# Kernel tuning notes

Measured on AMD Instinct MI355X. Metric: run time of the kernel, lower is better.

The kernel has to match this reference:

```python
import jax, jax.numpy as jnp
import numpy as np

NEG_INF = -1e30  # stand-in for -inf that stays stable under softmax


def setup_inputs() -> dict:
    key = jax.random.key(0)
    kk, kq, kv, ko = jax.random.split(key, 4)
    B, S, D = 4, 2048, 512
    return {
        "keys": jax.random.normal(kk, (B, S, D), dtype=jnp.float32),
        "queries": jax.random.normal(kq, (B, S, D), dtype=jnp.float32),
        "values": jax.random.normal(kv, (B, S, D), dtype=jnp.float32),
        "original": jax.random.normal(ko, (B, S, D), dtype=jnp.float32),
    }


def reference(keys, queries, values, original):
    # logits[b, i, j] = q[b, i, :] . k[b, j, :]  (no 1/sqrt(d) scaling in source)
    logits = jnp.einsum("bqd,bkd->bqk", queries, keys)
    S = logits.shape[-1]
    # causal mask: -inf strictly above the diagonal (triu, k=1)
    causal = jnp.tril(jnp.ones((S, S), dtype=bool))  # True where allowed
    logits = jnp.where(causal[None, :, :], logits, NEG_INF)
    probs = jax.nn.softmax(logits, axis=-1)
    read = jnp.einsum("bqk,bkd->bqd", probs, values)
    return jnp.concatenate([original, read], axis=-1)  # [B, S, 2D]
```

## Files before the change

### kernel.cpp

```cpp
#include <hip/hip_runtime.h>
#include <stdint.h>

#define BB 4
#define SS 2048
#define DD 512
#define NTQ 32
#define NEG_BIG -1e30f
#define RESC_THR 4.0f
#define CAPOUT 256

typedef __attribute__((ext_vector_type(4))) float f32x4;
typedef __attribute__((ext_vector_type(8))) _Float16 f16x8;
typedef __attribute__((ext_vector_type(4))) _Float16 f16x4;

typedef __attribute__((address_space(1))) void GV;
typedef __attribute__((address_space(3))) void LV;

union PK4 { _Float16 h[4]; uint2 u; };

__device__ __host__ __forceinline__ int rt_of(int t, int CC) {
  return (4 * (t + 1) + CC - 1) / CC;
}

__device__ __forceinline__ char* slot_base(float* Out, char* wsOp, int s, int& stride) {
  if (s < CAPOUT) { stride = 4096; return (char*)Out + (size_t)s * 131072; }
  stride = 2048;  return wsOp + (size_t)(s - CAPOUT) * 65536;
}

__global__ __launch_bounds__(256)
void prep_kernel(const float* __restrict__ K, const float* __restrict__ V,
                 char* __restrict__ PREP)
{
  const int blk = blockIdx.x;
  const int b   = blk >> 7;
  const int j   = blk & 127;
  const int tid = threadIdx.x;
  char* img = PREP + (size_t)blk * 32768;

  #pragma unroll
  for (int i = 0; i < 8; ++i) {
    int chunk = tid + 256 * i;
    int rr = chunk >> 7;
    int cc = (chunk & 127) << 2;
    float4 a = *(const float4*)(K + ((size_t)(b * SS + j * 16 + rr)) * DD + cc);
    PK4 p; p.h[0] = (_Float16)a.x; p.h[1] = (_Float16)a.y;
           p.h[2] = (_Float16)a.z; p.h[3] = (_Float16)a.w;
    int off = rr * 1024 + ((cc * 2) ^ ((rr & 7) << 4));
    *(uint2*)(img + off) = p.u;
  }

  #pragma unroll
  for (int half = 0; half < 2; ++half) {
    int d = tid + 256 * half;
    const float* vp = V + ((size_t)(b * SS + j * 16)) * DD + d;
    int e = d >> 5, mm = d & 15, p = (d >> 4) & 1;
    #pragma unroll
    for (int kq4 = 0; kq4 < 4; ++kq4) {
      PK4 pk;
      pk.h[0] = (_Float16)vp[(kq4 * 4 + 0) * DD];
      pk.h[1] = (_Float16)vp[(kq4 * 4 + 1) * DD];
      pk.h[2] = (_Float16)vp[(kq4 * 4 + 2) * DD];
      pk.h[3] = (_Float16)vp[(kq4 * 4 + 3) * DD];
      int slot = (kq4 ^ (mm & 3)) & 3;
      *(uint2*)(img + 16384 + e * 1024 + mm * 64 + slot * 16 + p * 8) = pk.u;
    }
  }
}

__global__ __launch_bounds__(256, 2)
void attn_kernel(const char* __restrict__ PREP, const float* __restrict__ Qg,
                 char* __restrict__ wsOp, float* __restrict__ MLp,
                 float* __restrict__ Out, int CC, int TSLOT)
{
  __shared__ char smem[2][32768];

  const int tid = threadIdx.x;
  const int ln  = tid & 63;
  const int w   = tid >> 6;
  const int m   = ln & 15;
  const int g   = ln >> 4;

  int t = 0, b = 0, r = 0;
  {
    int u = blockIdx.x, base = 0;
    for (int tt = NTQ - 1; tt >= 0; --tt) {
      int rt = rt_of(tt, CC);
      int cnt = BB * rt;
      if (u < base + cnt) { int loc = u - base; t = tt; r = loc / BB; b = loc % BB; break; }
      base += cnt;
    }
  }
  const int Rt     = rt_of(t, CC);
  const int direct = (Rt == 1);

  const int T16 = 4 * (t + 1);
  const int j0  = r * CC;
  const int j1  = min(j0 + CC, T16);
  const int nt  = j1 - j0;

  int slot = 0;
  if (!direct) {
    int off = 0;
    for (int tt = 0; tt < t; ++tt) {
      int rt = rt_of(tt, CC);
      if (rt >= 2) off += rt;
    }
    slot = b * TSLOT + off + r;
  }

  const int qrow  = t * 64 + w * 16 + m;
  const int qmaxw = t * 64 + w * 16 + 15;

  f16x8 qf[16];
  {
    const float* qp = Qg + ((size_t)(b * SS + qrow)) * DD + g * 8;
    #pragma unroll
    for (int ks = 0; ks < 16; ++ks) {
      float4 a0 = *(const float4*)(qp + ks * 32);
      float4 a1 = *(const float4*)(qp + ks * 32 + 4);
      f16x8 v;
      v[0] = (_Float16)a0.x; v[1] = (_Float16)a0.y;
      v[2] = (_Float16)a0.z; v[3] = (_Float16)a0.w;
      v[4] = (_Float16)a1.x; v[5] = (_Float16)a1.y;
      v[6] = (_Float16)a1.z; v[7] = (_Float16)a1.w;
      qf[ks] = v;
    }
  }

  f32x4 acc[32];
  {
    f32x4 z = {0.f, 0.f, 0.f, 0.f};
    #pragma unroll
    for (int i = 0; i < 32; ++i) acc[i] = z;
  }
  float mst = NEG_BIG, lst = 0.f;

  const char* tilebase = PREP + (size_t)b * 128 * 32768;

  auto STAGE = [&](int bi, int jt) {
    const char* src = tilebase + (size_t)jt * 32768;
    #pragma unroll
    for (int i = 0; i < 8; ++i) {
      int o = (tid + i * 256) * 16;
      __builtin_amdgcn_global_load_lds((GV*)(src + o), (LV*)(smem[bi] + o),
                                       16, 0, 0);
    }
  };

  STAGE(0, j0);

  const int vs = ((g ^ (m & 3)) & 3) * 16;

  for (int jj = 0; jj < nt; ++jj) {
    const int cur = jj & 1;
    __syncthreads();
    if (jj + 1 < nt) STAGE(cur ^ 1, j0 + jj + 1);

    const int kv0 = (j0 + jj) * 16;
    if (kv0 <= qmaxw) {
      const char* kb = smem[cur];

      f32x4 s0 = {0.f, 0.f, 0.f, 0.f};
      f32x4 s1 = {0.f, 0.f, 0.f, 0.f};
      {
        const char* krow = kb + m * 1024;
        const int rsw = (m & 7) << 4;
        __builtin_amdgcn_s_setprio(1);
        #pragma unroll
        for (int kk = 0; kk < 8; ++kk) {
          int offA = ((2 * kk) * 64 + g * 16) ^ rsw;
          int offB = ((2 * kk + 1) * 64 + g * 16) ^ rsw;
          f16x8 ka = *(const f16x8*)(krow + offA);
          f16x8 kb2 = *(const f16x8*)(krow + offB);
          s0 = __builtin_amdgcn_mfma_f32_16x16x32_f16(ka,  qf[2 * kk],     s0, 0, 0, 0);
          s1 = __builtin_amdgcn_mfma_f32_16x16x32_f16(kb2, qf[2 * kk + 1], s1, 0, 0, 0);
        }
        __builtin_amdgcn_s_setprio(0);
      }
      f32x4 s;
      s[0] = s0[0] + s1[0]; s[1] = s0[1] + s1[1];
      s[2] = s0[2] + s1[2]; s[3] = s0[3] + s1[3];

      float sv0 = (kv0 + 4 * g + 0 <= qrow) ? s[0] : NEG_BIG;
      float sv1 = (kv0 + 4 * g + 1 <= qrow) ? s[1] : NEG_BIG;
      float sv2 = (kv0 + 4 * g + 2 <= qrow) ? s[2] : NEG_BIG;
      float sv3 = (kv0 + 4 * g + 3 <= qrow) ? s[3] : NEG_BIG;
      float tm = fmaxf(fmaxf(sv0, sv1), fmaxf(sv2, sv3));
      tm = fmaxf(tm, __shfl_xor(tm, 16));
      tm = fmaxf(tm, __shfl_xor(tm, 32));

      float sc = 1.f;
      unsigned long long need = __ballot(tm > mst + RESC_THR);
      if (need) {
        float mnew = fmaxf(mst, tm);
        sc = __expf(mst - mnew);
        mst = mnew;
        #pragma unroll
        for (int i = 0; i < 32; ++i) {
          acc[i][0] *= sc; acc[i][1] *= sc; acc[i][2] *= sc; acc[i][3] *= sc;
        }
      }
      float p0 = (kv0 + 4 * g + 0 <= qrow) ? __expf(sv0 - mst) : 0.f;
      float p1 = (kv0 + 4 * g + 1 <= qrow) ? __expf(sv1 - mst) : 0.f;
      float p2 = (kv0 + 4 * g + 2 <= qrow) ? __expf(sv2 - mst) : 0.f;
      float p3 = (kv0 + 4 * g + 3 <= qrow) ? __expf(sv3 - mst) : 0.f;
      float rs = p0 + p1 + p2 + p3;
      rs += __shfl_xor(rs, 16);
      rs += __shfl_xor(rs, 32);
      lst = lst * sc + rs;

      f16x4 pf;
      pf[0] = (_Float16)p0; pf[1] = (_Float16)p1;
      pf[2] = (_Float16)p2; pf[3] = (_Float16)p3;
      const char* vb = kb + 16384;
      __builtin_amdgcn_s_setprio(1);
      #pragma unroll
      for (int e = 0; e < 16; ++e) {
        f16x8 vv = *(const f16x8*)(vb + e * 1024 + m * 64 + vs);
        f16x4 vlo; vlo[0] = vv[0]; vlo[1] = vv[1]; vlo[2] = vv[2]; vlo[3] = vv[3];
        f16x4 vhi; vhi[0] = vv[4]; vhi[1] = vv[5]; vhi[2] = vv[6]; vhi[3] = vv[7];
        acc[2 * e]     = __builtin_amdgcn_mfma_f32_16x16x16f16(vlo, pf, acc[2 * e],     0, 0, 0);
        acc[2 * e + 1] = __builtin_amdgcn_mfma_f32_16x16x16f16(vhi, pf, acc[2 * e + 1], 0, 0, 0);
      }
      __builtin_amdgcn_s_setprio(0);
    }
  }

  if (direct) {
    float inv = 1.0f / lst;
    float* orow = Out + ((size_t)(b * SS + qrow)) * 1024 + 512;
    #pragma unroll
    for (int dt = 0; dt < 32; ++dt) {
      float4 v4;
      v4.x = acc[dt][0] * inv; v4.y = acc[dt][1] * inv;
      v4.z = acc[dt][2] * inv; v4.w = acc[dt][3] * inv;
      *(float4*)(orow + dt * 16 + g * 4) = v4;
    }
  } else {
    const int q = w * 16 + m;
    if (ln < 16) {
      float* mlp = MLp + ((size_t)slot * 64 + q) * 2;
      mlp[0] = mst; mlp[1] = lst;
    }
    int stride; char* sb = slot_base(Out, wsOp, slot, stride);
    char* rowb = sb + (size_t)(q >> 1) * stride + (q & 1) * 1024;
    #pragma unroll
    for (int dt = 0; dt < 32; ++dt) {
      PK4 p;
      p.h[0] = (_Float16)acc[dt][0]; p.h[1] = (_Float16)acc[dt][1];
      p.h[2] = (_Float16)acc[dt][2]; p.h[3] = (_Float16)acc[dt][3];
      *(uint2*)(rowb + dt * 32 + g * 8) = p.u;
    }
  }
}

__global__ __launch_bounds__(256)
void combine_kernel(char* __restrict__ wsOp, const float* __restrict__ MLp,
                    float* __restrict__ Out, int CC, int TSLOT)
{
  int gid = blockIdx.x * 256 + threadIdx.x;
  int row = gid >> 7;
  int c4  = (gid & 127) << 2;
  int b = row >> 11;
  int s = row & 2047;
  int t = s >> 6;
  int qloc = s & 63;

  const int Rt = rt_of(t, CC);
  if (Rt < 2) return;

  int off = 0;
  for (int tt = 0; tt < t; ++tt) {
    int rt = rt_of(tt, CC);
    if (rt >= 2) off += rt;
  }
  const int base = b * TSLOT + off;

  float mr[8], lr[8];
  #pragma unroll
  for (int rr = 0; rr < 8; ++rr) { mr[rr] = NEG_BIG; lr[rr] = 0.f; }
  #pragma unroll
  for (int rr = 0; rr < 8; ++rr) {
    if (rr < Rt) {
      const float* p = MLp + ((size_t)(base + rr) * 64 + qloc) * 2;
      mr[rr] = p[0]; lr[rr] = p[1];
    }
  }
  float M = NEG_BIG;
  #pragma unroll
  for (int rr = 0; rr < 8; ++rr) M = fmaxf(M, mr[rr]);

  float L = 0.f, a0 = 0.f, a1 = 0.f, a2 = 0.f, a3 = 0.f;
  #pragma unroll
  for (int rr = 0; rr < 8; ++rr) {
    if (rr < Rt && mr[rr] > -5e29f) {
      float wgt = __expf(mr[rr] - M);
      L += wgt * lr[rr];
      int stride; char* sb = slot_base(Out, wsOp, base + rr, stride);
      const char* op = sb + (size_t)(qloc >> 1) * stride + (qloc & 1) * 1024 + c4 * 2;
      f16x4 ov = *(const f16x4*)op;
      a0 += wgt * (float)ov[0]; a1 += wgt * (float)ov[1];
      a2 += wgt * (float)ov[2]; a3 += wgt * (float)ov[3];
    }
  }
  float inv = 1.0f / L;
  float4 r4; r4.x = a0 * inv; r4.y = a1 * inv; r4.z = a2 * inv; r4.w = a3 * inv;
  *(float4*)(Out + (size_t)row * 1024 + 512 + c4) = r4;
}

__global__ __launch_bounds__(256)
void copy_orig(const float* __restrict__ orig, float* __restrict__ Out)
{
  int gid = blockIdx.x * 256 + threadIdx.x;
  int row = gid >> 7;
  int c4  = (gid & 127) << 2;
  *(float4*)(Out + (size_t)row * 1024 + c4) = *(const float4*)(orig + (size_t)row * 512 + c4);
}

extern "C" void kernel_launch(void* const* d_in, const int* in_sizes, int n_in,
                              void* d_out, int out_size, void* d_ws, size_t ws_size,
                              hipStream_t stream)
{
  (void)in_sizes; (void)n_in; (void)out_size;
  const float* keys     = (const float*)d_in[0];
  const float* queries  = (const float*)d_in[1];
  const float* values   = (const float*)d_in[2];
  const float* original = (const float*)d_in[3];
  float* out = (float*)d_out;

  const size_t PREPB = (size_t)BB * 128 * 32768;
  const size_t MLRES = 512 * 512;

  long nWs = (ws_size > PREPB + MLRES) ? (long)((ws_size - PREPB - MLRES) / 65536) : 0;
  long cap = CAPOUT + nWs;

  const int CCcand[8] = {20, 24, 28, 32, 40, 48, 64, 128};
  int CC = 128, TSLOT = 0, units = NTQ;
  for (int i = 0; i < 8; ++i) {
    int cc = CCcand[i];
    int un = 0, sl = 0;
    for (int t = 0; t < NTQ; ++t) {
      int rt = rt_of(t, cc);
      un += rt;
      if (rt >= 2) sl += rt;
    }
    long total = (long)BB * sl;
    if (total <= cap && total <= 512) { CC = cc; TSLOT = sl; units = un; break; }
  }

  char* PREP = (char*)d_ws;
  float* MLp = (float*)(PREP + PREPB);
  char* wsOp = PREP + PREPB + MLRES;

  hipLaunchKernelGGL(prep_kernel, dim3(BB * 128), dim3(256), 0, stream,
                     keys, values, PREP);

  hipLaunchKernelGGL(attn_kernel, dim3(BB * units), dim3(256), 0, stream,
                     PREP, queries, wsOp, MLp, out, CC, TSLOT);

  const int cgrid = (BB * SS * 128) / 256;
  hipLaunchKernelGGL(combine_kernel, dim3(cgrid), dim3(256), 0, stream,
                     wsOp, MLp, out, CC, TSLOT);
  hipLaunchKernelGGL(copy_orig, dim3(cgrid), dim3(256), 0, stream, original, out);
}
```

Measured before the change: 97.17 us.

## Fuse original copy into combine and store split partials in-place in output rows

Folds the copy of the original tensor into the combine kernel, so one launch writes both halves of each output row. Each row is now handled by a wavefront reading 8 fp16 partials per lane. The first four split partials per row are staged as fp16 inside that row's own 4 KB output region, with extra splits spilling to workspace. This lets smaller split sizes (CC down to 14) give more attention blocks. The aim is to cut a kernel launch and a pass over memory and to balance causal work better, at the cost of more partial traffic and extra combine work for rows with many splits.

```diff
diff --git a/kernel.cpp b/kernel.cpp
--- a/kernel.cpp
+++ b/kernel.cpp
@@ -7,7 +7,7 @@
 #define NTQ 32
 #define NEG_BIG -1e30f
 #define RESC_THR 4.0f
-#define CAPOUT 256
+#define MAXR 12
 
 typedef __attribute__((ext_vector_type(4))) float f32x4;
 typedef __attribute__((ext_vector_type(8))) _Float16 f16x8;
@@ -20,11 +20,6 @@
 
 __device__ __host__ __forceinline__ int rt_of(int t, int CC) {
   return (4 * (t + 1) + CC - 1) / CC;
-}
-
-__device__ __forceinline__ char* slot_base(float* Out, char* wsOp, int s, int& stride) {
-  if (s < CAPOUT) { stride = 4096; return (char*)Out + (size_t)s * 131072; }
-  stride = 2048;  return wsOp + (size_t)(s - CAPOUT) * 65536;
 }
 
 __global__ __launch_bounds__(256)
@@ -70,7 +65,7 @@
 __global__ __launch_bounds__(256, 2)
 void attn_kernel(const char* __restrict__ PREP, const float* __restrict__ Qg,
                  char* __restrict__ wsOp, float* __restrict__ MLp,
-                 float* __restrict__ Out, int CC, int TSLOT)
+                 float* __restrict__ Out, int CC, int TU, int WSB)
 {
   __shared__ char smem[2][32768];
 
@@ -97,16 +92,6 @@
   const int j0  = r * CC;
   const int j1  = min(j0 + CC, T16);
   const int nt  = j1 - j0;
-
-  int slot = 0;
-  if (!direct) {
-    int off = 0;
-    for (int tt = 0; tt < t; ++tt) {
-      int rt = rt_of(tt, CC);
-      if (rt >= 2) off += rt;
-    }
-    slot = b * TSLOT + off + r;
-  }
 
   const int qrow  = t * 64 + w * 16 + m;
   const int qmaxw = t * 64 + w * 16 + 15;
@@ -226,6 +211,7 @@
     }
   }
 
+  const int q = w * 16 + m;
   if (direct) {
     float inv = 1.0f / lst;
     float* orow = Out + ((size_t)(b * SS + qrow)) * 1024 + 512;
@@ -237,13 +223,23 @@
       *(float4*)(orow + dt * 16 + g * 4) = v4;
     }
   } else {
-    const int q = w * 16 + m;
+    int uoff = 0, wsoff = 0;
+    for (int tt = 0; tt < t; ++tt) {
+      int rtt = rt_of(tt, CC);
+      if (rtt >= 2) uoff += rtt;
+      if (rtt > 4)  wsoff += rtt - 4;
+    }
     if (ln < 16) {
-      float* mlp = MLp + ((size_t)slot * 64 + q) * 2;
+      float* mlp = MLp + ((size_t)(b * TU + uoff + r) * 64 + q) * 2;
       mlp[0] = mst; mlp[1] = lst;
     }
-    int stride; char* sb = slot_base(Out, wsOp, slot, stride);
-    char* rowb = sb + (size_t)(q >> 1) * stride + (q & 1) * 1024;
+    char* rowb;
+    if (r < 4) {
+      int hoff = (r & 2) ? ((r & 1) * 1024) : (2048 + (r & 1) * 1024);
+      rowb = (char*)Out + (size_t)(b * SS + t * 64 + q) * 4096 + hoff;
+    } else {
+      rowb = wsOp + ((size_t)(b * WSB + wsoff + (r - 4)) * 64 + q) * 1024;
+    }
     #pragma unroll
     for (int dt = 0; dt < 32; ++dt) {
       PK4 p;
@@ -255,66 +251,75 @@
 }
 
 __global__ __launch_bounds__(256)
-void combine_kernel(char* __restrict__ wsOp, const float* __restrict__ MLp,
-                    float* __restrict__ Out, int CC, int TSLOT)
+void combine_kernel(const char* __restrict__ wsOp, const float* __restrict__ MLp,
+                    const float* __restrict__ orig, float* Out,
+                    int CC, int TU, int WSB)
 {
-  int gid = blockIdx.x * 256 + threadIdx.x;
-  int row = gid >> 7;
-  int c4  = (gid & 127) << 2;
-  int b = row >> 11;
-  int s = row & 2047;
-  int t = s >> 6;
-  int qloc = s & 63;
+  const int row = blockIdx.x * 4 + (threadIdx.x >> 6);
+  const int ln  = threadIdx.x & 63;
+  const int b = row >> 11;
+  const int s = row & 2047;
+  const int t = s >> 6;
+  const int q = s & 63;
+  const int c0 = ln * 8;
+
+  const float* op = orig + (size_t)row * 512 + c0;
+  float4 og0 = *(const float4*)op;
+  float4 og1 = *(const float4*)(op + 4);
 
   const int Rt = rt_of(t, CC);
-  if (Rt < 2) return;
-
-  int off = 0;
-  for (int tt = 0; tt < t; ++tt) {
-    int rt = rt_of(tt, CC);
-    if (rt >= 2) off += rt;
-  }
-  const int base = b * TSLOT + off;
-
-  float mr[8], lr[8];
-  #pragma unroll
-  for (int rr = 0; rr < 8; ++rr) { mr[rr] = NEG_BIG; lr[rr] = 0.f; }
-  #pragma unroll
-  for (int rr = 0; rr < 8; ++rr) {
-    if (rr < Rt) {
-      const float* p = MLp + ((size_t)(base + rr) * 64 + qloc) * 2;
-      mr[rr] = p[0]; lr[rr] = p[1];
-    }
-  }
-  float M = NEG_BIG;
-  #pragma unroll
-  for (int rr = 0; rr < 8; ++rr) M = fmaxf(M, mr[rr]);
-
-  float L = 0.f, a0 = 0.f, a1 = 0.f, a2 = 0.f, a3 = 0.f;
-  #pragma unroll
-  for (int rr = 0; rr < 8; ++rr) {
-    if (rr < Rt && mr[rr] > -5e29f) {
-      float wgt = __expf(mr[rr] - M);
-      L += wgt * lr[rr];
-      int stride; char* sb = slot_base(Out, wsOp, base + rr, stride);
-      const char* op = sb + (size_t)(qloc >> 1) * stride + (qloc & 1) * 1024 + c4 * 2;
-      f16x4 ov = *(const f16x4*)op;
-      a0 += wgt * (float)ov[0]; a1 += wgt * (float)ov[1];
-      a2 += wgt * (float)ov[2]; a3 += wgt * (float)ov[3];
-    }
-  }
-  float inv = 1.0f / L;
-  float4 r4; r4.x = a0 * inv; r4.y = a1 * inv; r4.z = a2 * inv; r4.w = a3 * inv;
-  *(float4*)(Out + (size_t)row * 1024 + 512 + c4) = r4;
-}
-
-__global__ __launch_bounds__(256)
-void copy_orig(const float* __restrict__ orig, float* __restrict__ Out)
-{
-  int gid = blockIdx.x * 256 + threadIdx.x;
-  int row = gid >> 7;
-  int c4  = (gid & 127) << 2;
-  *(float4*)(Out + (size_t)row * 1024 + c4) = *(const float4*)(orig + (size_t)row * 512 + c4);
+  if (Rt >= 2) {
+    int uoff = 0, wsoff = 0;
+    for (int tt = 0; tt < t; ++tt) {
+      int rtt = rt_of(tt, CC);
+      if (rtt >= 2) uoff += rtt;
+      if (rtt > 4)  wsoff += rtt - 4;
+    }
+    float mr[MAXR], lr[MAXR];
+    #pragma unroll
+    for (int rr = 0; rr < MAXR; ++rr) { mr[rr] = NEG_BIG; lr[rr] = 0.f; }
+    #pragma unroll
+    for (int rr = 0; rr < MAXR; ++rr) {
+      if (rr < Rt) {
+        const float* p = MLp + ((size_t)(b * TU + uoff + rr) * 64 + q) * 2;
+        mr[rr] = p[0]; lr[rr] = p[1];
+      }
+    }
+    float M = NEG_BIG;
+    #pragma unroll
+    for (int rr = 0; rr < MAXR; ++rr) M = fmaxf(M, mr[rr]);
+
+    float L = 0.f;
+    float o[8];
+    #pragma unroll
+    for (int e = 0; e < 8; ++e) o[e] = 0.f;
+
+    #pragma unroll
+    for (int rr = 0; rr < MAXR; ++rr) {
+      if (rr < Rt) {
+        float wgt = __expf(mr[rr] - M);
+        L += wgt * lr[rr];
+        const char* sp;
+        if (rr < 4) {
+          int hoff = (rr & 2) ? ((rr & 1) * 1024) : (2048 + (rr & 1) * 1024);
+          sp = (const char*)Out + (size_t)row * 4096 + hoff + c0 * 2;
+        } else {
+          sp = wsOp + ((size_t)(b * WSB + wsoff + (rr - 4)) * 64 + q) * 1024 + c0 * 2;
+        }
+        f16x8 v = *(const f16x8*)sp;
+        #pragma unroll
+        for (int e = 0; e < 8; ++e) o[e] += wgt * (float)v[e];
+      }
+    }
+    float inv = 1.0f / L;
+    float4 r0, r1;
+    r0.x = o[0] * inv; r0.y = o[1] * inv; r0.z = o[2] * inv; r0.w = o[3] * inv;
+    r1.x = o[4] * inv; r1.y = o[5] * inv; r1.z = o[6] * inv; r1.w = o[7] * inv;
+    *(float4*)(Out + (size_t)row * 1024 + 512 + c0)     = r0;
+    *(float4*)(Out + (size_t)row * 1024 + 512 + c0 + 4) = r1;
+  }
+  *(float4*)(Out + (size_t)row * 1024 + c0)     = og0;
+  *(float4*)(Out + (size_t)row * 1024 + c0 + 4) = og1;
 }
 
 extern "C" void kernel_launch(void* const* d_in, const int* in_sizes, int n_in,
@@ -329,37 +334,32 @@
   float* out = (float*)d_out;
 
   const size_t PREPB = (size_t)BB * 128 * 32768;
-  const size_t MLRES = 512 * 512;
-
-  long nWs = (ws_size > PREPB + MLRES) ? (long)((ws_size - PREPB - MLRES) / 65536) : 0;
-  long cap = CAPOUT + nWs;
-
-  const int CCcand[8] = {20, 24, 28, 32, 40, 48, 64, 128};
-  int CC = 128, TSLOT = 0, units = NTQ;
-  for (int i = 0; i < 8; ++i) {
+
+  const int CCcand[7] = {14, 15, 16, 20, 24, 32, 128};
+  int CC = 128, TU = 0, WSB = 0, units = NTQ;
+  for (int i = 0; i < 7; ++i) {
     int cc = CCcand[i];
-    int un = 0, sl = 0;
+    int tu = 0, wsb = 0, un = 0;
     for (int t = 0; t < NTQ; ++t) {
       int rt = rt_of(t, cc);
       un += rt;
-      if (rt >= 2) sl += rt;
-    }
-    long total = (long)BB * sl;
-    if (total <= cap && total <= 512) { CC = cc; TSLOT = sl; units = un; break; }
+      if (rt >= 2) tu += rt;
+      if (rt > 4)  wsb += rt - 4;
+    }
+    size_t need = PREPB + (size_t)BB * tu * 512 + (size_t)BB * wsb * 65536;
+    if (ws_size >= need) { CC = cc; TU = tu; WSB = wsb; units = un; break; }
   }
 
   char* PREP = (char*)d_ws;
   float* MLp = (float*)(PREP + PREPB);
-  char* wsOp = PREP + PREPB + MLRES;
+  char* wsOp = PREP + PREPB + (size_t)BB * TU * 512;
 
   hipLaunchKernelGGL(prep_kernel, dim3(BB * 128), dim3(256), 0, stream,
                      keys, values, PREP);
 
   hipLaunchKernelGGL(attn_kernel, dim3(BB * units), dim3(256), 0, stream,
-                     PREP, queries, wsOp, MLp, out, CC, TSLOT);
-
-  const int cgrid = (BB * SS * 128) / 256;
-  hipLaunchKernelGGL(combine_kernel, dim3(cgrid), dim3(256), 0, stream,
-                     wsOp, MLp, out, CC, TSLOT);
-  hipLaunchKernelGGL(copy_orig, dim3(cgrid), dim3(256), 0, stream, original, out);
-}
+                     PREP, queries, wsOp, MLp, out, CC, TU, WSB);
+
+  hipLaunchKernelGGL(combine_kernel, dim3((BB * SS) / 4), dim3(256), 0, stream,
+                     wsOp, MLp, original, out, CC, TU, WSB);
+}
```

After: 110.4 us. +13.7%, slower.
